# Kernel tuning notes

Measured on AMD Instinct MI355X. Metric: run time of the kernel, lower is better.

## Reference

```python
import jax, jax.numpy as jnp
import numpy as np
from jax import lax

B, T, E, H, A, V = 128, 64, 512, 512, 512, 10000


def setup_inputs() -> dict:
    key = jax.random.key(0)
    ks = jax.random.split(key, 16)
    # lengths: descending, in [1, T], first forced to T (pack_padded_sequence requirement)
    ln = np.asarray(jax.random.randint(ks[0], (B,), 1, T + 1))
    ln = np.sort(ln)[::-1].copy()
    ln[0] = T
    u = lambda k, s, a=0.1: jax.random.uniform(k, s, jnp.float32, -a, a)
    return {
        "features": jax.random.normal(ks[1], (B, E), jnp.float32),
        "captions": jax.random.randint(ks[2], (B, T - 1), 0, V),
        "lengths": jnp.asarray(ln, jnp.int64) if jax.config.jax_enable_x64 else jnp.asarray(ln, jnp.int32),
        "cnn_features": jax.random.normal(ks[3], (B, A), jnp.float32),
        "emb_W": u(ks[4], (V, E)),
        "W_ih": u(ks[5], (4 * H, E), 1.0 / np.sqrt(H)),
        "W_hh": u(ks[6], (4 * H, H), 1.0 / np.sqrt(H)),
        "b_ih": u(ks[7], (4 * H,), 1.0 / np.sqrt(H)),
        "b_hh": u(ks[8], (4 * H,), 1.0 / np.sqrt(H)),
        "att_W": u(ks[9], (A, H + E)),
        "att_b": jnp.zeros((A,), jnp.float32),
        "attd_W": u(ks[10], (E, A + E)),
        "attd_b": jnp.zeros((E,), jnp.float32),
        "out_W": u(ks[11], (V, H)),
        "out_b": jnp.zeros((V,), jnp.float32),
    }


def _lstm_cell(x, h, c, W_ih, W_hh, b_ih, b_hh):
    g = x @ W_ih.T + b_ih + h @ W_hh.T + b_hh  # (B, 4H)
    i, f, gg, o = jnp.split(g, 4, axis=-1)
    i = jax.nn.sigmoid(i); f = jax.nn.sigmoid(f)
    gg = jnp.tanh(gg); o = jax.nn.sigmoid(o)
    c2 = f * c + i * gg
    return o * jnp.tanh(c2), c2


def reference(features, captions, lengths, cnn_features, emb_W, W_ih, W_hh, b_ih, b_hh,
              att_W, att_b, attd_W, attd_b, out_W, out_b):
    emb = emb_W[captions]                                    # (B, T-1, E)
    xs = jnp.concatenate([features[:, None, :], emb], 1)     # (B, T, E)
    h0 = jnp.zeros((B, H), xs.dtype)
    c0 = jnp.zeros((B, H), xs.dtype)
    # step 0: plain LSTM on raw input, zero initial state (all sequences active)
    h1, c1 = _lstm_cell(xs[:, 0], h0, c0, W_ih, W_hh, b_ih, b_hh)

    def step(carry, inp):
        h, c = carry
        x, t = inp                                           # x: (B, E)
        aw = jax.nn.softmax(jnp.concatenate([x, h], 1) @ att_W.T + att_b, axis=1)
        attended = cnn_features * aw                         # (B, A)
        x2 = jnp.concatenate([x, attended], 1) @ attd_W.T + attd_b  # (B, E)
        h2, c2 = _lstm_cell(x2, h, c, W_ih, W_hh, b_ih, b_hh)
        active = (t < lengths)[:, None]
        h = jnp.where(active, h2, h)
        c = jnp.where(active, c2, c)
        return (h, c), jnp.where(active, h2, jnp.zeros_like(h2))

    xs_t = jnp.swapaxes(xs[:, 1:], 0, 1)                     # (T-1, B, E)
    _, outs = lax.scan(step, (h1, c1), (xs_t, jnp.arange(1, T)))
    hidden = jnp.concatenate([h1[None], outs], 0)            # (T, B, H)
    logits = hidden @ out_W.T + out_b                        # (T, B, V)
    valid = (jnp.arange(T)[:, None] < lengths[None, :])      # (T, B)
    return jnp.where(valid[:, :, None], logits, jnp.zeros_like(logits))
```

## Files before the change

kernel.cpp:

```cpp
#include <hip/hip_runtime.h>
#include <hip/hip_bf16.h>

#define B 128
#define T 64
#define E 512
#define H 512
#define AA 512
#define V 10000

typedef __hip_bfloat16 bf16;
typedef unsigned long long u64;
typedef unsigned short u16;
typedef __attribute__((ext_vector_type(8))) short bf16x8s;
typedef __attribute__((ext_vector_type(4))) float f32x4;

#define MFMA __builtin_amdgcn_mfma_f32_16x16x32_bf16

__device__ __forceinline__ bf16x8s ld8(const bf16* p) {
  return *reinterpret_cast<const bf16x8s*>(p);
}
__device__ __forceinline__ float sigm(float x) { return 1.f / (1.f + __expf(-x)); }
__device__ __forceinline__ float bf2f(u16 u) {
  return __uint_as_float(((unsigned)u) << 16);
}


__global__ __launch_bounds__(256) void kxs(const float* __restrict__ feat,
                                           const int* __restrict__ cap,
                                           const float* __restrict__ embW,
                                           bf16* __restrict__ xs) {
  int idx = blockIdx.x * 256 + threadIdx.x;
  int e4 = (idx & 127) << 2;
  int b = (idx >> 7) & 127;
  int t = idx >> 14;
  const float* src = (t == 0) ? (feat + (size_t)b * E)
                              : (embW + (size_t)cap[b * (T - 1) + (t - 1)] * E);
  float4 v = *reinterpret_cast<const float4*>(src + e4);
  bf16* d = xs + ((size_t)t * B + b) * E + e4;
  d[0] = __float2bfloat16(v.x); d[1] = __float2bfloat16(v.y);
  d[2] = __float2bfloat16(v.z); d[3] = __float2bfloat16(v.w);
}

__global__ __launch_bounds__(256) void kcast(const float* __restrict__ s,
                                             bf16* __restrict__ d, int n4) {
  int i = blockIdx.x * 256 + threadIdx.x;
  if (i >= n4) return;
  float4 v = *reinterpret_cast<const float4*>(s + (size_t)i * 4);
  d[i * 4 + 0] = __float2bfloat16(v.x); d[i * 4 + 1] = __float2bfloat16(v.y);
  d[i * 4 + 2] = __float2bfloat16(v.z); d[i * 4 + 3] = __float2bfloat16(v.w);
}

__global__ __launch_bounds__(256) void kslice(const float* __restrict__ src,
                                              bf16* __restrict__ dst, int c0) {
  int i = blockIdx.x * 256 + threadIdx.x;
  int row = i >> 7, c4 = (i & 127) << 2;
  float4 v = *reinterpret_cast<const float4*>(src + (size_t)row * 1024 + c0 + c4);
  bf16* d = dst + (size_t)row * 512 + c4;
  d[0] = __float2bfloat16(v.x); d[1] = __float2bfloat16(v.y);
  d[2] = __float2bfloat16(v.z); d[3] = __float2bfloat16(v.w);
}

__global__ __launch_bounds__(256) void ktrans(const float* __restrict__ src,
                                              bf16* __restrict__ dst, int coff) {
  __shared__ float tl[32][33];
  int bx = blockIdx.x & 15, by = blockIdx.x >> 4;
  int tx = threadIdx.x & 31, ty = threadIdx.x >> 5;
  for (int yy = ty; yy < 32; yy += 8)
    tl[yy][tx] = src[(size_t)(by * 32 + yy) * 1024 + coff + bx * 32 + tx];
  __syncthreads();
  for (int yy = ty; yy < 32; yy += 8)
    dst[(size_t)(bx * 32 + yy) * 512 + by * 32 + tx] = __float2bfloat16(tl[tx][yy]);
}

__global__ __launch_bounds__(256) void kpadW(const float* __restrict__ s,
                                             bf16* __restrict__ d) {
  int i = blockIdx.x * 256 + threadIdx.x;
  int row = (i << 2) / H;
  float4 v = make_float4(0.f, 0.f, 0.f, 0.f);
  if (row < V) v = *reinterpret_cast<const float4*>(s + (size_t)i * 4);
  d[i * 4 + 0] = __float2bfloat16(v.x); d[i * 4 + 1] = __float2bfloat16(v.y);
  d[i * 4 + 2] = __float2bfloat16(v.z); d[i * 4 + 3] = __float2bfloat16(v.w);
}

__global__ __launch_bounds__(256) void kgb(const float* __restrict__ bih,
                                           const float* __restrict__ bhh,
                                           const float* __restrict__ Wih_f,
                                           const float* __restrict__ attdb,
                                           float* __restrict__ gb0,
                                           float* __restrict__ gbA) {
  int g = blockIdx.x * 256 + threadIdx.x;
  if (g >= 2048) return;
  float b0 = bih[g] + bhh[g];
  float s = 0.f;
  for (int e = 0; e < 512; ++e) s += Wih_f[(size_t)g * 512 + e] * attdb[e];
  gb0[g] = b0; gbA[g] = b0 + s;
}

__global__ __launch_bounds__(512) void kpack(const u16* __restrict__ Gx,
                                             const u16* __restrict__ Sxb,
                                             u16* __restrict__ Gxp,
                                             u16* __restrict__ Sxp) {
  int bid = blockIdx.x;
  int t = bid >> 5, wid = bid & 31;
  int tid = threadIdx.x;
  int w = tid >> 6, lane = tid & 63;
  int fr = lane & 15, fq = lane >> 4;
  int r0 = w * 16 + fq * 4;
  int cb = wid << 4;
  u16 g[16], s[4];
  #pragma unroll
  for (int q = 0; q < 4; ++q)
    #pragma unroll
    for (int j = 0; j < 4; ++j)
      g[q * 4 + j] = Gx[((size_t)t * B + r0 + j) * 2048 + q * 512 + cb + fr];
  #pragma unroll
  for (int j = 0; j < 4; ++j)
    s[j] = Sxb[((size_t)t * B + r0 + j) * AA + cb + fr];
  size_t ob = ((size_t)bid * 512 + tid);
  #pragma unroll
  for (int k = 0; k < 16; ++k) Gxp[ob * 16 + k] = g[k];
  #pragma unroll
  for (int j = 0; j < 4; ++j) Sxp[ob * 4 + j] = s[j];
}

__global__ __launch_bounds__(256) void kgemm(const bf16* __restrict__ Ag,
                                             const bf16* __restrict__ Bg,
                                             const float* __restrict__ bias,
                                             bf16* __restrict__ outB,
                                             int nbn, int Nld) {
  __shared__ __align__(16) char lds[2][2][16384];
  const int nwg = gridDim.x;
  const int bid0 = blockIdx.x;
  const int wg = (bid0 & 7) * (nwg >> 3) + (bid0 >> 3);
  const int bm = wg / nbn, bn = wg % nbn;
  const int tid = threadIdx.x, w = tid >> 6, lane = tid & 63;
  const int fr = lane & 15, fq = lane >> 4, ko = fq << 3;
  const int mh = w >> 1, nh = w & 1;
  const bf16* Abase = Ag + (size_t)bm * 128 * 512;
  const bf16* Bbase = Bg + (size_t)bn * 128 * 512;
  f32x4 acc[4][4] = {};
  auto STAGE = [&](int buf, int k0) {
    #pragma unroll
    for (int m = 0; m < 2; ++m) {
      const bf16* base = m ? Bbase : Abase;
      #pragma unroll
      for (int it = 0; it < 4; ++it) {
        int si = tid + it * 256;
        int row = si >> 3;
        int s = (si & 7) ^ (row & 7);
        __builtin_amdgcn_global_load_lds(
          (const __attribute__((address_space(1))) void*)(base + (size_t)row * 512 + k0 + s * 8),
          (__attribute__((address_space(3))) void*)(&lds[buf][m][((tid & ~63) + it * 256) * 16]),
          16, 0, 0);
      }
    }
  };
  STAGE(0, 0);
  __syncthreads();
  for (int kt = 0; kt < 8; ++kt) {
    int cur = kt & 1;
    if (kt < 7) STAGE(cur ^ 1, (kt + 1) * 64);
    #pragma unroll
    for (int kk = 0; kk < 64; kk += 32) {
      bf16x8s a[4], b[4];
      #pragma unroll
      for (int i = 0; i < 4; ++i) {
        int ra = mh * 64 + i * 16 + fr;
        a[i] = *reinterpret_cast<const bf16x8s*>(
            &lds[cur][0][ra * 128 + ((((kk + ko) >> 3) ^ (ra & 7)) << 4)]);
        int rb = nh * 64 + i * 16 + fr;
        b[i] = *reinterpret_cast<const bf16x8s*>(
            &lds[cur][1][rb * 128 + ((((kk + ko) >> 3) ^ (rb & 7)) << 4)]);
      }
      #pragma unroll
      for (int mi = 0; mi < 4; ++mi)
        #pragma unroll
        for (int ni = 0; ni < 4; ++ni)
          acc[mi][ni] = MFMA(a[mi], b[ni], acc[mi][ni], 0, 0, 0);
    }
    __syncthreads();
  }
  #pragma unroll
  for (int mi = 0; mi < 4; ++mi)
    #pragma unroll
    for (int ni = 0; ni < 4; ++ni)
      #pragma unroll
      for (int j = 0; j < 4; ++j) {
        int row = bm * 128 + mh * 64 + mi * 16 + fq * 4 + j;
        int col = bn * 128 + nh * 64 + ni * 16 + fr;
        float bv = bias ? bias[col] : 0.f;
        outB[(size_t)row * Nld + col] = __float2bfloat16(acc[mi][ni][j] + bv);
      }
}

__global__ __launch_bounds__(256, 4) void kfinal(const bf16* __restrict__ Ag,
                                                 const bf16* __restrict__ Bg,
                                                 const float* __restrict__ bias,
                                                 const int* __restrict__ len,
                                                 float* __restrict__ out) {
  __shared__ __align__(16) char lds[2][2][8192];
  const int nwg = gridDim.x;
  const int bid0 = blockIdx.x;
  const int wg = (bid0 & 7) * (nwg >> 3) + (bid0 >> 3);
  const int bm = wg / 79, bn = wg % 79;
  const int tid = threadIdx.x, w = tid >> 6, lane = tid & 63;
  const int fr = lane & 15, fq = lane >> 4;
  const int mh = w >> 1, nh = w & 1;
  const bf16* Abase = Ag + (size_t)bm * 128 * 512;
  const bf16* Bbase = Bg + (size_t)bn * 128 * 512;
  f32x4 acc[4][4] = {};
  auto STAGE = [&](int buf, int k0) {
    #pragma unroll
    for (int m = 0; m < 2; ++m) {
      const bf16* base = m ? Bbase : Abase;
      #pragma unroll
      for (int it = 0; it < 2; ++it) {
        int u = it * 256 + tid;
        int row = u >> 2, c = u & 3;
        int cs = c ^ ((row >> 1) & 3);
        __builtin_amdgcn_global_load_lds(
          (const __attribute__((address_space(1))) void*)(base + (size_t)row * 512 + k0 + cs * 8),
          (__attribute__((address_space(3))) void*)(&lds[buf][m][((tid & ~63) + it * 256) * 16]),
          16, 0, 0);
      }
    }
  };
  STAGE(0, 0);
  __syncthreads();
  for (int kt = 0; kt < 16; ++kt) {
    int cur = kt & 1;
    if (kt < 15) STAGE(cur ^ 1, (kt + 1) * 32);
    bf16x8s a[4], b[4];
    #pragma unroll
    for (int i = 0; i < 4; ++i) {
      int ra = mh * 64 + i * 16 + fr;
      a[i] = *reinterpret_cast<const bf16x8s*>(
          &lds[cur][0][ra * 64 + ((fq ^ ((ra >> 1) & 3)) << 4)]);
      int rb = nh * 64 + i * 16 + fr;
      b[i] = *reinterpret_cast<const bf16x8s*>(
          &lds[cur][1][rb * 64 + ((fq ^ ((rb >> 1) & 3)) << 4)]);
    }
    #pragma unroll
    for (int mi = 0; mi < 4; ++mi)
      #pragma unroll
      for (int ni = 0; ni < 4; ++ni)
        acc[mi][ni] = MFMA(a[mi], b[ni], acc[mi][ni], 0, 0, 0);
    __syncthreads();
  }
  #pragma unroll
  for (int mi = 0; mi < 4; ++mi)
    #pragma unroll
    for (int ni = 0; ni < 4; ++ni)
      #pragma unroll
      for (int j = 0; j < 4; ++j) {
        int row = bm * 128 + mh * 64 + mi * 16 + fq * 4 + j;
        int col = bn * 128 + nh * 64 + ni * 16 + fr;
        if (col < V) {
          int tt = row >> 7, bb = row & 127;
          out[(size_t)row * V + col] = (tt < len[bb]) ? acc[mi][ni][j] + bias[col] : 0.f;
        }
      }
}

__global__ __launch_bounds__(512, 1) void kloop(
    const u16* __restrict__ Sxp,
    const u16* __restrict__ Gxp,
    const bf16* __restrict__ Kc,
    const bf16* __restrict__ Whh,
    const bf16* __restrict__ WaH,
    const float* __restrict__ gb0,
    const float* __restrict__ gbA,
    const float* __restrict__ cnn,
    const int* __restrict__ len,
    bf16* __restrict__ hstore,
    bf16* __restrict__ pstore,
    float* __restrict__ Zbuf,
    bf16* __restrict__ hid,
    int* ticket, int* winner, int* flags) {
  __shared__ __align__(16) char KcS[65536];
  __shared__ __align__(16) char WhS[65536];
  __shared__ __align__(16) char WaS[16384];
  __shared__ int steam[2];

  if (threadIdx.x == 0) {
    int xcc;
    asm volatile("s_getreg_b32 %0, hwreg(HW_REG_XCC_ID)" : "=s"(xcc));
    xcc &= 15;
    int my = __hip_atomic_fetch_add(&ticket[xcc], 1, __ATOMIC_RELAXED,
                                    __HIP_MEMORY_SCOPE_AGENT);
    if (my == 31) {
      int exp = -1;
      __hip_atomic_compare_exchange_strong(winner, &exp, xcc, __ATOMIC_RELAXED,
                                           __ATOMIC_RELAXED, __HIP_MEMORY_SCOPE_AGENT);
    }
    int wv;
    while ((wv = __hip_atomic_load(winner, __ATOMIC_RELAXED,
                                   __HIP_MEMORY_SCOPE_AGENT)) < 0)
      __builtin_amdgcn_s_sleep(8);
    steam[0] = (wv == xcc && my < 32) ? 1 : 0;
    steam[1] = my;
  }
  __syncthreads();
  if (!steam[0]) return;
  const int wid = steam[1];

  const int tid = threadIdx.x, w = tid >> 6, lane = tid & 63;
  const int fr = lane & 15, fq = lane >> 4, ko = fq << 3;
  const int cb = wid << 4;
  const int col = cb + fr;

  for (int u = tid; u < 4096; u += 512) {
    int row = u >> 6, chunk = u & 63;
    int g = (row >> 4) * 512 + cb + (row & 15);
    int off = row * 1024 + ((chunk ^ (row & 7)) << 4);
    *reinterpret_cast<bf16x8s*>(&KcS[off]) = ld8(Kc + (size_t)g * 512 + chunk * 8);
    *reinterpret_cast<bf16x8s*>(&WhS[off]) = ld8(Whh + (size_t)g * 512 + chunk * 8);
  }
  for (int u = tid; u < 1024; u += 512) {
    int row = u >> 6, chunk = u & 63;
    *reinterpret_cast<bf16x8s*>(&WaS[row * 1024 + ((chunk ^ (row & 7)) << 4)]) =
        ld8(WaH + (size_t)(cb + row) * 512 + chunk * 8);
  }

  const int r0 = w * 16 + fq * 4;
  int4 lv4 = *reinterpret_cast<const int4*>(len + r0);
  int lv[4] = {lv4.x, lv4.y, lv4.z, lv4.w};
  float cnnv[4], gb0v[4], gbAv[4];
  #pragma unroll
  for (int j = 0; j < 4; ++j) cnnv[j] = cnn[(size_t)(r0 + j) * AA + col];
  #pragma unroll
  for (int q = 0; q < 4; ++q) {
    gb0v[q] = gb0[q * 512 + col];
    gbAv[q] = gbA[q * 512 + col];
  }
  float cstv[4] = {0.f, 0.f, 0.f, 0.f};
  u16 hpv[4] = {0, 0, 0, 0};
  __syncthreads();

  auto arrive = [&](int ep2) {
    __syncthreads();
    if (tid == 0)
      __hip_atomic_store(flags + wid * 16, ep2, __ATOMIC_RELAXED,
                         __HIP_MEMORY_SCOPE_AGENT);
  };
  auto wait = [&](int ep2) {
    if (tid < 64) {
      const int* fp = flags + (tid & 31) * 16;
      while (__ballot(__hip_atomic_load(fp, __ATOMIC_RELAXED,
                                        __HIP_MEMORY_SCOPE_AGENT) < ep2))
        __builtin_amdgcn_s_sleep(1);
    }
    __syncthreads();
  };

  int ep = 0;
  for (int t = 0; t < T; ++t) {
    if (t) { ++ep; arrive(ep); }
    size_t pb = ((size_t)(t * 32 + wid) * 512 + tid);
    u64 gw[4];
    const u64* gp = reinterpret_cast<const u64*>(Gxp) + pb * 4;
    #pragma unroll
    for (int k = 0; k < 4; ++k) gw[k] = __builtin_nontemporal_load(gp + k);
    u64 sw = 0;
    if (t) sw = __builtin_nontemporal_load(reinterpret_cast<const u64*>(Sxp) + pb);
    const bf16* hin = hstore + (size_t)(t ? t - 1 : 0) * B * H;
    bf16* pst = pstore + (size_t)t * B * AA;
    f32x4 accH[4] = {}, accP[4] = {};
    if (t) {
      wait(ep);
      bf16x8s a_h[16];
      {
        const bf16* ha = hin + (size_t)(w * 16 + fr) * H + ko;
        #pragma unroll
        for (int i = 0; i < 16; ++i) a_h[i] = ld8(ha + i * 32);
      }
      f32x4 acc1 = {};
      #pragma unroll
      for (int k = 0; k < 512; k += 32) {
        bf16x8s b = *reinterpret_cast<const bf16x8s*>(
            &WaS[fr * 1024 + ((((k >> 3) + fq) ^ (fr & 7)) << 4)]);
        acc1 = MFMA(a_h[k >> 5], b, acc1, 0, 0, 0);
      }
      float pj[4];
      #pragma unroll
      for (int j = 0; j < 4; ++j) {
        pj[j] = __expf(acc1[j] + bf2f((u16)(sw >> (16 * j))));
        bf16 pb2 = __float2bfloat16(pj[j] * cnnv[j]);
        pst[(size_t)(r0 + j) * AA + col] = pb2;
      }
      #pragma unroll
      for (int j = 0; j < 4; ++j) {
        float z = pj[j];
        z += __shfl_xor(z, 1); z += __shfl_xor(z, 2);
        z += __shfl_xor(z, 4); z += __shfl_xor(z, 8);
        if (fr == 0)
          __hip_atomic_fetch_add(Zbuf + t * B + r0 + j, z, __ATOMIC_RELAXED,
                                 __HIP_MEMORY_SCOPE_WORKGROUP);
      }
      ++ep; arrive(ep);
      #pragma unroll 2
      for (int k = 0; k < 512; k += 32) {
        bf16x8s a = a_h[k >> 5];
        #pragma unroll
        for (int q = 0; q < 4; ++q) {
          bf16x8s b = *reinterpret_cast<const bf16x8s*>(
              &WhS[(q * 16 + fr) * 1024 + ((((k >> 3) + fq) ^ (fr & 7)) << 4)]);
          accH[q] = MFMA(a, b, accH[q], 0, 0, 0);
        }
      }
      wait(ep);
      {
        const bf16* pa = pst + (size_t)(w * 16 + fr) * AA + ko;
        #pragma unroll 2
        for (int k = 0; k < 512; k += 32) {
          bf16x8s a = ld8(pa + k);
          #pragma unroll
          for (int q = 0; q < 4; ++q) {
            bf16x8s b = *reinterpret_cast<const bf16x8s*>(
                &KcS[(q * 16 + fr) * 1024 + ((((k >> 3) + fq) ^ (fr & 7)) << 4)]);
            accP[q] = MFMA(a, b, accP[q], 0, 0, 0);
          }
        }
      }
      float4 zv = *reinterpret_cast<const float4*>(Zbuf + t * B + r0);
      float zp[4] = {zv.x, zv.y, zv.z, zv.w};
      #pragma unroll
      for (int q = 0; q < 4; ++q)
        #pragma unroll
        for (int j = 0; j < 4; ++j)
          accP[q][j] *= __fdividef(1.f, zp[j]);
    }
    float gsel[4];
    #pragma unroll
    for (int q = 0; q < 4; ++q) gsel[q] = t ? gbAv[q] : gb0v[q];
    #pragma unroll
    for (int j = 0; j < 4; ++j) {
      float gi = sigm(accP[0][j] + accH[0][j] + gsel[0] + bf2f((u16)(gw[0] >> (16 * j))));
      float gf = sigm(accP[1][j] + accH[1][j] + gsel[1] + bf2f((u16)(gw[1] >> (16 * j))));
      float gg = tanhf(accP[2][j] + accH[2][j] + gsel[2] + bf2f((u16)(gw[2] >> (16 * j))));
      float go = sigm(accP[3][j] + accH[3][j] + gsel[3] + bf2f((u16)(gw[3] >> (16 * j))));
      float c2 = gf * cstv[j] + gi * gg;
      float h2 = go * tanhf(c2);
      bool act = t < lv[j];
      if (act) cstv[j] = c2;
      bf16 hb = __float2bfloat16(h2);
      u16 hbits = *reinterpret_cast<u16*>(&hb);
      hpv[j] = act ? hbits : hpv[j];
      ((u16*)hstore)[((size_t)t * B + r0 + j) * H + col] = hpv[j];
      ((u16*)hid)[((size_t)t * B + r0 + j) * H + col] = act ? hbits : (u16)0;
    }
  }
}


extern "C" void kernel_launch(void* const* d_in, const int* in_sizes, int n_in,
                              void* d_out, int out_size, void* d_ws, size_t ws_size,
                              hipStream_t stream) {
  const float* feat   = (const float*)d_in[0];
  const int*   cap    = (const int*)d_in[1];
  const int*   len    = (const int*)d_in[2];
  const float* cnn    = (const float*)d_in[3];
  const float* embW   = (const float*)d_in[4];
  const float* Wih_f  = (const float*)d_in[5];
  const float* Whh_f  = (const float*)d_in[6];
  const float* bih    = (const float*)d_in[7];
  const float* bhh    = (const float*)d_in[8];
  const float* attW_f = (const float*)d_in[9];
  const float* attb   = (const float*)d_in[10];
  const float* attdW_f= (const float*)d_in[11];
  const float* attdb  = (const float*)d_in[12];
  const float* outW_f = (const float*)d_in[13];
  const float* outb   = (const float*)d_in[14];
  float* out = (float*)d_out;
  char* ws = (char*)d_ws;

  size_t off = 0;
  auto alloc = [&](size_t n) { char* p = ws + off; off += (n + 255) & ~(size_t)255; return p; };
  bf16*  xs    = (bf16*)alloc(8388608);
  bf16*  WaX   = (bf16*)alloc(524288);
  bf16*  WaH   = (bf16*)alloc(524288);
  bf16*  WdXT  = (bf16*)alloc(524288);
  bf16*  WdAT  = (bf16*)alloc(524288);
  bf16*  Wihb  = (bf16*)alloc(2097152);
  bf16*  Whhb  = (bf16*)alloc(2097152);
  bf16*  Kc    = (bf16*)alloc(2097152);
  bf16*  outWp = (bf16*)alloc(10354688);
  bf16*  Sxb   = (bf16*)alloc(8388608);
  bf16*  Gx    = (bf16*)alloc(33554432);
  u16*   Gxp   = (u16*)alloc(33554432);
  u16*   Sxp   = (u16*)alloc(8388608);
  bf16*  hid   = (bf16*)alloc(8388608);
  bf16*  hstore= (bf16*)alloc(8388608);
  bf16*  pstore= (bf16*)alloc(8388608);
  float* gb0   = (float*)alloc(8192);
  float* gbA   = (float*)alloc(8192);
  float* Zbuf  = (float*)alloc(32768);
  int*   ticket= (int*)alloc(256);
  int*   winner= (int*)alloc(256);
  int*   flags = (int*)alloc(2048);
  bf16*  Kx    = pstore;

  kxs<<<4096, 256, 0, stream>>>(feat, cap, embW, xs);
  kslice<<<256, 256, 0, stream>>>(attW_f, WaX, 0);
  kslice<<<256, 256, 0, stream>>>(attW_f, WaH, 512);
  ktrans<<<256, 256, 0, stream>>>(attdW_f, WdXT, 0);
  ktrans<<<256, 256, 0, stream>>>(attdW_f, WdAT, 512);
  kcast<<<1024, 256, 0, stream>>>(Wih_f, Wihb, 262144);
  kcast<<<1024, 256, 0, stream>>>(Whh_f, Whhb, 262144);
  kpadW<<<5056, 256, 0, stream>>>(outW_f, outWp);
  kgb<<<8, 256, 0, stream>>>(bih, bhh, Wih_f, attdb, gb0, gbA);

  kgemm<<<256, 256, 0, stream>>>(xs, WaX, attb, Sxb, 4, 512);
  kgemm<<<64, 256, 0, stream>>>(Wihb, WdXT, nullptr, Kx, 4, 512);
  kgemm<<<64, 256, 0, stream>>>(Wihb, WdAT, nullptr, Kc, 4, 512);
  kgemm<<<1024, 256, 0, stream>>>(xs, Kx, nullptr, Gx, 16, 2048);
  kgemm<<<16, 256, 0, stream>>>(xs, Wihb, nullptr, Gx, 16, 2048);

  kpack<<<2048, 512, 0, stream>>>((const u16*)Gx, (const u16*)Sxb, Gxp, Sxp);

  hipMemsetAsync(ticket, 0, 256, stream);
  hipMemsetAsync(winner, 0xFF, 256, stream);
  hipMemsetAsync(flags, 0, 2048, stream);
  hipMemsetAsync(Zbuf, 0, 32768, stream);

  kloop<<<256, 512, 0, stream>>>(Sxp, Gxp, Kc, Whhb, WaH, gb0, gbA, cnn, len,
                                 hstore, pstore, Zbuf, hid, ticket, winner, flags);

  kfinal<<<5056, 256, 0, stream>>>(hid, outWp, outb, len, out);
}
```

Before: 1.780 ms.

## Switch recurrent loop GEMMs to 32x32 MFMA with LDS gate exchange

The recurrent kernel's h·Whh and p·Kc products now use 32x32x16 MFMA tiles, each wave computing a 32x32 block. The results are staged through an LDS gateX buffer and remapped to a per-thread row/column layout for the LSTM elementwise update, and kpack's Gx packing is changed to match. The attention projection now reads WaH directly from global memory instead of caching it in LDS, which frees LDS for the gate buffer. The hidden-state register preload is removed. The aim is denser MFMA use with fewer instructions per step, at the cost of extra __syncthreads and LDS traffic on the serial critical path.

```diff
diff --git a/kernel.cpp b/kernel.cpp
--- a/kernel.cpp
+++ b/kernel.cpp
@@ -1,5 +1,6 @@
 #include <hip/hip_runtime.h>
 #include <hip/hip_bf16.h>
+#include <limits.h>
 
 #define B 128
 #define T 64
@@ -13,8 +14,10 @@
 typedef unsigned short u16;
 typedef __attribute__((ext_vector_type(8))) short bf16x8s;
 typedef __attribute__((ext_vector_type(4))) float f32x4;
+typedef __attribute__((ext_vector_type(16))) float f32x16;
 
 #define MFMA __builtin_amdgcn_mfma_f32_16x16x32_bf16
+#define MFMA32 __builtin_amdgcn_mfma_f32_32x32x16_bf16
 
 __device__ __forceinline__ bf16x8s ld8(const bf16* p) {
   return *reinterpret_cast<const bf16x8s*>(p);
@@ -102,25 +105,28 @@
                                              u16* __restrict__ Sxp) {
   int bid = blockIdx.x;
   int t = bid >> 5, wid = bid & 31;
+  int cb = wid << 4;
   int tid = threadIdx.x;
-  int w = tid >> 6, lane = tid & 63;
-  int fr = lane & 15, fq = lane >> 4;
-  int r0 = w * 16 + fq * 4;
-  int cb = wid << 4;
-  u16 g[16], s[4];
-  #pragma unroll
-  for (int q = 0; q < 4; ++q)
+  {
+    int ccol = tid & 15, rb = (tid >> 4) * 4;
+    u16 g[16];
+    #pragma unroll
+    for (int q = 0; q < 4; ++q)
+      #pragma unroll
+      for (int j = 0; j < 4; ++j)
+        g[q * 4 + j] = Gx[((size_t)t * B + rb + j) * 2048 + q * 512 + cb + ccol];
+    u16* dst = Gxp + ((size_t)bid * 512 + tid) * 16;
+    #pragma unroll
+    for (int k = 0; k < 16; ++k) dst[k] = g[k];
+  }
+  {
+    int w = tid >> 6, lane = tid & 63;
+    int fr = lane & 15, fq = lane >> 4;
     #pragma unroll
     for (int j = 0; j < 4; ++j)
-      g[q * 4 + j] = Gx[((size_t)t * B + r0 + j) * 2048 + q * 512 + cb + fr];
-  #pragma unroll
-  for (int j = 0; j < 4; ++j)
-    s[j] = Sxb[((size_t)t * B + r0 + j) * AA + cb + fr];
-  size_t ob = ((size_t)bid * 512 + tid);
-  #pragma unroll
-  for (int k = 0; k < 16; ++k) Gxp[ob * 16 + k] = g[k];
-  #pragma unroll
-  for (int j = 0; j < 4; ++j) Sxp[ob * 4 + j] = s[j];
+      Sxp[((size_t)bid * 512 + tid) * 4 + j] =
+          Sxb[((size_t)t * B + w * 16 + fq * 4 + j) * AA + cb + fr];
+  }
 }
 
 __global__ __launch_bounds__(256) void kgemm(const bf16* __restrict__ Ag,
@@ -277,10 +283,10 @@
     float* __restrict__ Zbuf,
     bf16* __restrict__ hid,
     int* ticket, int* winner, int* flags) {
+  __shared__ __align__(16) char WhS[65536];
   __shared__ __align__(16) char KcS[65536];
-  __shared__ __align__(16) char WhS[65536];
-  __shared__ __align__(16) char WaS[16384];
-  __shared__ int steam[2];
+  __shared__ __align__(16) float gateX[128][64];
+  int* steam = reinterpret_cast<int*>(&gateX[0][0]);
 
   if (threadIdx.x == 0) {
     int xcc;
@@ -306,35 +312,33 @@
 
   const int tid = threadIdx.x, w = tid >> 6, lane = tid & 63;
   const int fr = lane & 15, fq = lane >> 4, ko = fq << 3;
-  const int cb = wid << 4;
-  const int col = cb + fr;
+  const int cb = wid << 4, col = cb + fr;
+  const int mt = w & 3, nt = w >> 2;
+  const int la = lane & 31, hi = lane >> 5;
+  const int p1r0 = w * 16 + fq * 4;
+  const int ccol = tid & 15, rb = (tid >> 4) * 4;
 
   for (int u = tid; u < 4096; u += 512) {
     int row = u >> 6, chunk = u & 63;
     int g = (row >> 4) * 512 + cb + (row & 15);
     int off = row * 1024 + ((chunk ^ (row & 7)) << 4);
+    *reinterpret_cast<bf16x8s*>(&WhS[off]) = ld8(Whh + (size_t)g * 512 + chunk * 8);
     *reinterpret_cast<bf16x8s*>(&KcS[off]) = ld8(Kc + (size_t)g * 512 + chunk * 8);
-    *reinterpret_cast<bf16x8s*>(&WhS[off]) = ld8(Whh + (size_t)g * 512 + chunk * 8);
-  }
-  for (int u = tid; u < 1024; u += 512) {
-    int row = u >> 6, chunk = u & 63;
-    *reinterpret_cast<bf16x8s*>(&WaS[row * 1024 + ((chunk ^ (row & 7)) << 4)]) =
-        ld8(WaH + (size_t)(cb + row) * 512 + chunk * 8);
-  }
-
-  const int r0 = w * 16 + fq * 4;
-  int4 lv4 = *reinterpret_cast<const int4*>(len + r0);
+  }
+  float cnnv[4];
+  #pragma unroll
+  for (int j = 0; j < 4; ++j) cnnv[j] = cnn[(size_t)(p1r0 + j) * AA + col];
+  int4 lv4 = *reinterpret_cast<const int4*>(len + rb);
   int lv[4] = {lv4.x, lv4.y, lv4.z, lv4.w};
-  float cnnv[4], gb0v[4], gbAv[4];
-  #pragma unroll
-  for (int j = 0; j < 4; ++j) cnnv[j] = cnn[(size_t)(r0 + j) * AA + col];
+  float gb0v[4], gbAv[4];
   #pragma unroll
   for (int q = 0; q < 4; ++q) {
-    gb0v[q] = gb0[q * 512 + col];
-    gbAv[q] = gbA[q * 512 + col];
+    gb0v[q] = gb0[q * 512 + cb + ccol];
+    gbAv[q] = gbA[q * 512 + cb + ccol];
   }
   float cstv[4] = {0.f, 0.f, 0.f, 0.f};
   u16 hpv[4] = {0, 0, 0, 0};
+  const bf16* WaB = WaH + (size_t)col * 512;
   __syncthreads();
 
   auto arrive = [&](int ep2) {
@@ -356,89 +360,96 @@
   int ep = 0;
   for (int t = 0; t < T; ++t) {
     if (t) { ++ep; arrive(ep); }
-    size_t pb = ((size_t)(t * 32 + wid) * 512 + tid);
+    const u64* gp = reinterpret_cast<const u64*>(Gxp) +
+                    ((size_t)(t * 32 + wid) * 512 + tid) * 4;
     u64 gw[4];
-    const u64* gp = reinterpret_cast<const u64*>(Gxp) + pb * 4;
     #pragma unroll
     for (int k = 0; k < 4; ++k) gw[k] = __builtin_nontemporal_load(gp + k);
     u64 sw = 0;
-    if (t) sw = __builtin_nontemporal_load(reinterpret_cast<const u64*>(Sxp) + pb);
+    if (t) sw = __builtin_nontemporal_load(
+        reinterpret_cast<const u64*>(Sxp) + (size_t)(t * 32 + wid) * 512 + tid);
     const bf16* hin = hstore + (size_t)(t ? t - 1 : 0) * B * H;
     bf16* pst = pstore + (size_t)t * B * AA;
-    f32x4 accH[4] = {}, accP[4] = {};
     if (t) {
       wait(ep);
-      bf16x8s a_h[16];
       {
         const bf16* ha = hin + (size_t)(w * 16 + fr) * H + ko;
+        f32x4 acc1 = {};
+        #pragma unroll 4
+        for (int k = 0; k < 512; k += 32)
+          acc1 = MFMA(ld8(ha + k), ld8(WaB + k + ko), acc1, 0, 0, 0);
+        float pj[4];
         #pragma unroll
-        for (int i = 0; i < 16; ++i) a_h[i] = ld8(ha + i * 32);
-      }
-      f32x4 acc1 = {};
-      #pragma unroll
-      for (int k = 0; k < 512; k += 32) {
-        bf16x8s b = *reinterpret_cast<const bf16x8s*>(
-            &WaS[fr * 1024 + ((((k >> 3) + fq) ^ (fr & 7)) << 4)]);
-        acc1 = MFMA(a_h[k >> 5], b, acc1, 0, 0, 0);
-      }
-      float pj[4];
-      #pragma unroll
-      for (int j = 0; j < 4; ++j) {
-        pj[j] = __expf(acc1[j] + bf2f((u16)(sw >> (16 * j))));
-        bf16 pb2 = __float2bfloat16(pj[j] * cnnv[j]);
-        pst[(size_t)(r0 + j) * AA + col] = pb2;
-      }
-      #pragma unroll
-      for (int j = 0; j < 4; ++j) {
-        float z = pj[j];
-        z += __shfl_xor(z, 1); z += __shfl_xor(z, 2);
-        z += __shfl_xor(z, 4); z += __shfl_xor(z, 8);
-        if (fr == 0)
-          __hip_atomic_fetch_add(Zbuf + t * B + r0 + j, z, __ATOMIC_RELAXED,
-                                 __HIP_MEMORY_SCOPE_WORKGROUP);
+        for (int j = 0; j < 4; ++j) {
+          pj[j] = __expf(acc1[j] + bf2f((u16)(sw >> (16 * j))));
+          bf16 pb2 = __float2bfloat16(pj[j] * cnnv[j]);
+          ((u16*)pst)[(size_t)(p1r0 + j) * AA + col] = *reinterpret_cast<u16*>(&pb2);
+        }
+        #pragma unroll
+        for (int j = 0; j < 4; ++j) {
+          float z = pj[j];
+          z += __shfl_xor(z, 1); z += __shfl_xor(z, 2);
+          z += __shfl_xor(z, 4); z += __shfl_xor(z, 8);
+          if (fr == 0)
+            __hip_atomic_fetch_add(Zbuf + t * B + p1r0 + j, z, __ATOMIC_RELAXED,
+                                   __HIP_MEMORY_SCOPE_WORKGROUP);
+        }
       }
       ++ep; arrive(ep);
-      #pragma unroll 2
-      for (int k = 0; k < 512; k += 32) {
-        bf16x8s a = a_h[k >> 5];
-        #pragma unroll
-        for (int q = 0; q < 4; ++q) {
+      f32x16 accH = {};
+      {
+        const bf16* ha = hin + (size_t)(32 * mt + la) * H + 8 * hi;
+        #pragma unroll 4
+        for (int kk = 0; kk < 32; ++kk) {
+          bf16x8s a = ld8(ha + 16 * kk);
+          int brow = 32 * nt + la;
+          int chunk = 2 * kk + hi;
           bf16x8s b = *reinterpret_cast<const bf16x8s*>(
-              &WhS[(q * 16 + fr) * 1024 + ((((k >> 3) + fq) ^ (fr & 7)) << 4)]);
-          accH[q] = MFMA(a, b, accH[q], 0, 0, 0);
+              &WhS[brow * 1024 + ((chunk ^ (brow & 7)) << 4)]);
+          accH = MFMA32(a, b, accH, 0, 0, 0);
         }
       }
       wait(ep);
+      f32x16 accP = {};
       {
-        const bf16* pa = pst + (size_t)(w * 16 + fr) * AA + ko;
-        #pragma unroll 2
-        for (int k = 0; k < 512; k += 32) {
-          bf16x8s a = ld8(pa + k);
-          #pragma unroll
-          for (int q = 0; q < 4; ++q) {
-            bf16x8s b = *reinterpret_cast<const bf16x8s*>(
-                &KcS[(q * 16 + fr) * 1024 + ((((k >> 3) + fq) ^ (fr & 7)) << 4)]);
-            accP[q] = MFMA(a, b, accP[q], 0, 0, 0);
-          }
+        const bf16* pa = pst + (size_t)(32 * mt + la) * AA + 8 * hi;
+        #pragma unroll 4
+        for (int kk = 0; kk < 32; ++kk) {
+          bf16x8s a = ld8(pa + 16 * kk);
+          int brow = 32 * nt + la;
+          int chunk = 2 * kk + hi;
+          bf16x8s b = *reinterpret_cast<const bf16x8s*>(
+              &KcS[brow * 1024 + ((chunk ^ (brow & 7)) << 4)]);
+          accP = MFMA32(a, b, accP, 0, 0, 0);
         }
       }
-      float4 zv = *reinterpret_cast<const float4*>(Zbuf + t * B + r0);
-      float zp[4] = {zv.x, zv.y, zv.z, zv.w};
-      #pragma unroll
-      for (int q = 0; q < 4; ++q)
-        #pragma unroll
-        for (int j = 0; j < 4; ++j)
-          accP[q][j] *= __fdividef(1.f, zp[j]);
-    }
-    float gsel[4];
-    #pragma unroll
-    for (int q = 0; q < 4; ++q) gsel[q] = t ? gbAv[q] : gb0v[q];
+      float zp[4][4];
+      #pragma unroll
+      for (int g = 0; g < 4; ++g) {
+        float4 zv = *reinterpret_cast<const float4*>(
+            Zbuf + t * B + 32 * mt + 8 * g + 4 * hi);
+        zp[g][0] = zv.x; zp[g][1] = zv.y; zp[g][2] = zv.z; zp[g][3] = zv.w;
+      }
+      #pragma unroll
+      for (int r = 0; r < 16; ++r) {
+        int m = (r & 3) + 8 * (r >> 2) + 4 * hi;
+        gateX[32 * mt + m][32 * nt + la] =
+            accH[r] + accP[r] * __fdividef(1.f, zp[r >> 2][r & 3]);
+      }
+    }
+    __syncthreads();
     #pragma unroll
     for (int j = 0; j < 4; ++j) {
-      float gi = sigm(accP[0][j] + accH[0][j] + gsel[0] + bf2f((u16)(gw[0] >> (16 * j))));
-      float gf = sigm(accP[1][j] + accH[1][j] + gsel[1] + bf2f((u16)(gw[1] >> (16 * j))));
-      float gg = tanhf(accP[2][j] + accH[2][j] + gsel[2] + bf2f((u16)(gw[2] >> (16 * j))));
-      float go = sigm(accP[3][j] + accH[3][j] + gsel[3] + bf2f((u16)(gw[3] >> (16 * j))));
+      int row = rb + j;
+      float z0 = 0.f, z1 = 0.f, z2 = 0.f, z3 = 0.f;
+      if (t) {
+        z0 = gateX[row][0 * 16 + ccol]; z1 = gateX[row][1 * 16 + ccol];
+        z2 = gateX[row][2 * 16 + ccol]; z3 = gateX[row][3 * 16 + ccol];
+      }
+      float gi = sigm(z0 + (t ? gbAv[0] : gb0v[0]) + bf2f((u16)(gw[0] >> (16 * j))));
+      float gf = sigm(z1 + (t ? gbAv[1] : gb0v[1]) + bf2f((u16)(gw[1] >> (16 * j))));
+      float gg = tanhf(z2 + (t ? gbAv[2] : gb0v[2]) + bf2f((u16)(gw[2] >> (16 * j))));
+      float go = sigm(z3 + (t ? gbAv[3] : gb0v[3]) + bf2f((u16)(gw[3] >> (16 * j))));
       float c2 = gf * cstv[j] + gi * gg;
       float h2 = go * tanhf(c2);
       bool act = t < lv[j];
@@ -446,9 +457,11 @@
       bf16 hb = __float2bfloat16(h2);
       u16 hbits = *reinterpret_cast<u16*>(&hb);
       hpv[j] = act ? hbits : hpv[j];
-      ((u16*)hstore)[((size_t)t * B + r0 + j) * H + col] = hpv[j];
-      ((u16*)hid)[((size_t)t * B + r0 + j) * H + col] = act ? hbits : (u16)0;
-    }
+      ((u16*)hstore)[((size_t)t * B + row) * H + cb + ccol] = hpv[j];
+      __builtin_nontemporal_store(act ? hbits : (u16)0,
+          (u16*)hid + ((size_t)t * B + row) * H + cb + ccol);
+    }
+    __syncthreads();
   }
 }
 
@@ -497,7 +510,7 @@
   float* Zbuf  = (float*)alloc(32768);
   int*   ticket= (int*)alloc(256);
   int*   winner= (int*)alloc(256);
-  int*   flags = (int*)alloc(2048);
+  int*   flags = (int*)alloc(4096);
   bf16*  Kx    = pstore;
 
   kxs<<<4096, 256, 0, stream>>>(feat, cap, embW, xs);
@@ -520,7 +533,7 @@
 
   hipMemsetAsync(ticket, 0, 256, stream);
   hipMemsetAsync(winner, 0xFF, 256, stream);
-  hipMemsetAsync(flags, 0, 2048, stream);
+  hipMemsetAsync(flags, 0, 4096, stream);
   hipMemsetAsync(Zbuf, 0, 32768, stream);
 
   kloop<<<256, 512, 0, stream>>>(Sxp, Gxp, Kc, Whhb, WaH, gb0, gbA, cnn, len,
```

After: 2.273 ms. 27.7% more time.
